# Optimization experiments

Measured on AMD Instinct MI355X. Metric: run time of the kernel, lower is better.

Reference implementation:

```python
import jax, jax.numpy as jnp
import numpy as np
import math

IN_DIM = 256
DQK = IN_DIM // 8


def setup_inputs() -> dict:
    key = jax.random.key(0)
    k = jax.random.split(key, 7)
    B, C, W = 4, IN_DIM, 4096
    x_0 = jax.random.normal(k[0], (B, C, W), dtype=jnp.float32)
    x_1 = jax.random.normal(k[1], (B, C, W), dtype=jnp.float32)
    s = 1.0 / math.sqrt(C)
    # 1x1 Conv1d == dense projection over channel dim: weight [out, in], bias [out]
    wq = jax.random.normal(k[2], (DQK, C), dtype=jnp.float32) * s
    bq = jax.random.normal(k[3], (DQK,), dtype=jnp.float32) * s
    wk = jax.random.normal(k[4], (DQK, C), dtype=jnp.float32) * s
    bk = jax.random.normal(k[5], (DQK,), dtype=jnp.float32) * s
    # torch init is zeros; use small random so the attention path contributes
    gamma = jax.random.normal(k[6], (1,), dtype=jnp.float32) * 0.1
    return {"x_0": x_0, "x_1": x_1, "wq": wq, "bq": bq, "wk": wk, "bk": bk, "gamma": gamma}


def reference(x_0, x_1, wq, bq, wk, bk, gamma):
    B, C, W0 = x_0.shape
    scale = 1.0 / math.sqrt(C)
    # 1x1 conv projections: [B, dqk, W]
    q = jnp.einsum('dc,bcw->bdw', wq, x_0) + bq[None, :, None]   # [B, dqk, W0]
    k = jnp.einsum('dc,bcw->bdw', wk, x_1) + bk[None, :, None]   # [B, dqk, W1]
    # energy = key^T @ query, scaled: [B, W1, W0]
    energy = jnp.einsum('bdm,bdn->bmn', k, q) * scale
    attention = jax.nn.softmax(energy, axis=-1)                  # softmax over W0
    # out = attention @ x_0^T -> [B, W1, C] -> permute to [B, C, W1]
    out = jnp.einsum('bmn,bcn->bcm', attention, x_0)
    out = gamma[0] * out + x_1
    return out, attention
```

## Files before the change

kernel.cpp:

```cpp
#include <hip/hip_runtime.h>
#include <stdint.h>

#define B_    4
#define C_    256
#define W_    4096
#define DQK_  32
#define NT64_ 64
#define TSZ_  16384

typedef short bf16x8 __attribute__((ext_vector_type(8)));
typedef float f32x4  __attribute__((ext_vector_type(4)));

__device__ __forceinline__ float fexp2f(float x){
#if __has_builtin(__builtin_amdgcn_exp2f)
  return __builtin_amdgcn_exp2f(x);
#else
  return exp2f(x);
#endif
}
__device__ __forceinline__ float frcpf(float x){
#if __has_builtin(__builtin_amdgcn_rcpf)
  return __builtin_amdgcn_rcpf(x);
#else
  return 1.0f / x;
#endif
}
__device__ __forceinline__ uint32_t cvtpk(float a, float b){
  uint32_t r;
  asm("v_cvt_pk_bf16_f32 %0, %1, %2" : "=v"(r) : "v"(a), "v"(b));
  return r;
}
__device__ __forceinline__ unsigned short bf16c(float f){
  return (unsigned short)cvtpk(f, f);
}

__global__ __launch_bounds__(512) void sa_prep(
    const float* __restrict__ x0, const float* __restrict__ x1,
    const float* __restrict__ wq, const float* __restrict__ bq,
    const float* __restrict__ wk, const float* __restrict__ bk,
    unsigned short* __restrict__ qf, unsigned short* __restrict__ kT,
    unsigned short* __restrict__ x0f)
{
  const int b    = blockIdx.y;
  const int nt   = blockIdx.x;
  const int tid  = threadIdx.x;
  const int lane = tid & 63;
  const int cq   = __builtin_amdgcn_readfirstlane(tid >> 6);
  const int n    = nt * 64 + lane;
  const int lr   = lane & 15, lg = lane >> 4;
  const size_t bw = (size_t)b * ((size_t)C_ * W_) + n;

  __shared__ union {
    unsigned short xs[256 * 68];
    float red[8][64][33];
  } sm;

  float accq[DQK_], acck[DQK_];
  #pragma unroll
  for (int d = 0; d < DQK_; ++d){ accq[d] = 0.f; acck[d] = 0.f; }

  const int c0 = cq * 32;
  for (int i = 0; i < 32; ++i){
    const int c = c0 + i;
    const size_t off = bw + (size_t)c * W_;
    const float v0 = x0[off];
    const float v1 = x1[off];
    sm.xs[c * 68 + lane] = bf16c(v0);
    #pragma unroll
    for (int d = 0; d < DQK_; ++d){
      accq[d] = fmaf(wq[d * C_ + c], v0, accq[d]);
      acck[d] = fmaf(wk[d * C_ + c], v1, acck[d]);
    }
  }

  {
    unsigned short* xt = x0f + (size_t)(b * NT64_ + nt) * TSZ_;
    #pragma unroll
    for (int ct = 0; ct < 2; ++ct)
      #pragma unroll
      for (int ks = 0; ks < 2; ++ks){
        uint4 v = *(const uint4*)&sm.xs[(c0 + ct * 16 + lr) * 68 + ks * 32 + lg * 8];
        *(uint4*)(xt + ((size_t)((cq * 2 + ct) * 2 + ks) * 64 + lane) * 8) = v;
      }
  }
  __syncthreads();

  #pragma unroll
  for (int d = 0; d < DQK_; ++d) sm.red[cq][lane][d] = accq[d];
  __syncthreads();
  {
    const int nl = tid & 63, dg = tid >> 6;
    const int d0 = dg * 4;
    float s[4];
    #pragma unroll
    for (int j = 0; j < 4; ++j){
      float t = bq[d0 + j];
      #pragma unroll
      for (int g = 0; g < 8; ++g) t += sm.red[g][nl][d0 + j];
      s[j] = t;
    }
    uint2 pk; pk.x = cvtpk(s[0], s[1]); pk.y = cvtpk(s[2], s[3]);
    const int ng = nt * 64 + nl;
    const size_t addr = (((size_t)b * 256 + (ng >> 4)) * 64
                         + (ng & 15) + ((dg >> 1) << 4)) * 8 + (dg & 1) * 4;
    *(uint2*)(qf + addr) = pk;
  }
  __syncthreads();

  #pragma unroll
  for (int d = 0; d < DQK_; ++d) sm.red[cq][lane][d] = acck[d];
  __syncthreads();
  {
    const float SCL = 0.0625f * 1.44269504088896340736f;
    const int nl = tid & 63, dg = tid >> 6;
    const int d0 = dg * 4;
    float s[4];
    #pragma unroll
    for (int j = 0; j < 4; ++j){
      float t = bk[d0 + j];
      #pragma unroll
      for (int g = 0; g < 8; ++g) t += sm.red[g][nl][d0 + j];
      s[j] = t * SCL;
    }
    uint2 pk; pk.x = cvtpk(s[0], s[1]); pk.y = cvtpk(s[2], s[3]);
    *(uint2*)(kT + ((size_t)b * W_ + nt * 64 + nl) * DQK_ + d0) = pk;
  }
}

__global__ __launch_bounds__(512, 2) void sa_fused(
    const unsigned short* __restrict__ qf, const unsigned short* __restrict__ kT,
    const unsigned short* __restrict__ x0f, const float* __restrict__ x1,
    const float* __restrict__ gamma,
    float* __restrict__ out, float* __restrict__ att)
{
  const int lb = blockIdx.x;
  const int b    = (lb & 7) >> 1;
  const int mblk = ((lb >> 3) << 1) | (lb & 1);
  const int m0 = mblk * 64;
  const int tid = threadIdx.x;
  const int lane = tid & 63;
  const int wid = tid >> 6;
  const int lr = lane & 15, lg = lane >> 4;
  const int nq = wid >> 1;
  const int mh = wid & 1;

  __shared__ __align__(16) unsigned short Plds[2][64 * 64];
  __shared__ float ssum[4][64];

  const int row0 = mh * 32 + lr, row1 = row0 + 16;
  const bf16x8 kf0 = *(const bf16x8*)(kT + ((size_t)b * W_ + m0 + row0) * DQK_ + lg * 8);
  const bf16x8 kf1 = *(const bf16x8*)(kT + ((size_t)b * W_ + m0 + row1) * DQK_ + lg * 8);
  const unsigned short* qfw = qf + ((size_t)b * 256 * 64 + (size_t)nq * 64 + lane) * 8;
  const unsigned short* afw = x0f + (size_t)b * NT64_ * TSZ_ + wid * 2048 + lane * 8;

  float ps0 = 0.f, ps1 = 0.f;
  {
    const unsigned short* qp = qfw + 2048;
    bf16x8 qv = *(const bf16x8*)qfw;
    for (int s = 0; s < NT64_; ++s){
      bf16x8 qn = *(const bf16x8*)qp;
      qp = (s == NT64_ - 2) ? qfw : (qp + 2048);
      f32x4 e0 = __builtin_amdgcn_mfma_f32_16x16x32_bf16(qv, kf0, (f32x4){0.f,0.f,0.f,0.f}, 0, 0, 0);
      f32x4 e1 = __builtin_amdgcn_mfma_f32_16x16x32_bf16(qv, kf1, (f32x4){0.f,0.f,0.f,0.f}, 0, 0, 0);
      ps0 += (fexp2f(e0[0]) + fexp2f(e0[1])) + (fexp2f(e0[2]) + fexp2f(e0[3]));
      ps1 += (fexp2f(e1[0]) + fexp2f(e1[1])) + (fexp2f(e1[2]) + fexp2f(e1[3]));
      qv = qn;
    }
  }
  ps0 += __shfl_xor(ps0, 16); ps0 += __shfl_xor(ps0, 32);
  ps1 += __shfl_xor(ps1, 16); ps1 += __shfl_xor(ps1, 32);
  if (lane < 16){
    ssum[nq][mh * 32 + lane]      = ps0;
    ssum[nq][mh * 32 + 16 + lane] = ps1;
  }
  __syncthreads();
  const float is0 = frcpf(ssum[0][row0] + ssum[1][row0] + ssum[2][row0] + ssum[3][row0]);
  const float is1 = frcpf(ssum[0][row1] + ssum[1][row1] + ssum[2][row1] + ssum[3][row1]);

  f32x4 acc[2][4];
  #pragma unroll
  for (int ct = 0; ct < 2; ++ct)
    #pragma unroll
    for (int m2 = 0; m2 < 4; ++m2) acc[ct][m2] = (f32x4){0.f,0.f,0.f,0.f};

  const int pw0 = row0 * 64 + (((nq * 2 + (lg >> 1)) ^ (row0 & 7)) << 3) + (lg & 1) * 4;
  const int pw1 = row1 * 64 + (((nq * 2 + (lg >> 1)) ^ (row1 & 7)) << 3) + (lg & 1) * 4;
  int pfo[4][2];
  #pragma unroll
  for (int m2 = 0; m2 < 4; ++m2){
    const int prow = m2 * 16 + lr;
    #pragma unroll
    for (int ks = 0; ks < 2; ++ks)
      pfo[m2][ks] = prow * 64 + (((ks * 4 + lg) ^ (prow & 7)) << 3);
  }

  const unsigned short* qp = qfw + 2048;
  const unsigned short* afp = afw + TSZ_;
  float* attw0 = att + ((size_t)b * W_ + m0 + row0) * W_ + nq * 16 + lg * 4;
  float* attw1 = attw0 + (size_t)16 * W_;

  bf16x8 qv = *(const bf16x8*)qfw;
  bf16x8 af0 = *(const bf16x8*)(afw);
  bf16x8 af1 = *(const bf16x8*)(afw + 512);
  bf16x8 af2 = *(const bf16x8*)(afw + 1024);
  bf16x8 af3 = *(const bf16x8*)(afw + 1536);

  for (int s = 0; s < NT64_; ++s){
    const int cur = s & 1;

    f32x4 e0 = __builtin_amdgcn_mfma_f32_16x16x32_bf16(qv, kf0, (f32x4){0.f,0.f,0.f,0.f}, 0, 0, 0);
    f32x4 e1 = __builtin_amdgcn_mfma_f32_16x16x32_bf16(qv, kf1, (f32x4){0.f,0.f,0.f,0.f}, 0, 0, 0);
    f32x4 p0, p1;
    #pragma unroll
    for (int r = 0; r < 4; ++r){
      p0[r] = fexp2f(e0[r]) * is0;
      p1[r] = fexp2f(e1[r]) * is1;
    }
    uint2 pv0; pv0.x = cvtpk(p0[0], p0[1]); pv0.y = cvtpk(p0[2], p0[3]);
    uint2 pv1; pv1.x = cvtpk(p1[0], p1[1]); pv1.y = cvtpk(p1[2], p1[3]);
    *(uint2*)(&Plds[cur][0] + pw0) = pv0;
    *(uint2*)(&Plds[cur][0] + pw1) = pv1;

    asm volatile("s_waitcnt lgkmcnt(0)" ::: "memory");
    __builtin_amdgcn_sched_barrier(0);
    __builtin_amdgcn_s_barrier();

    qv = *(const bf16x8*)qp;
    qp = (s == NT64_ - 2) ? qfw : (qp + 2048);
    bf16x8 an0 = *(const bf16x8*)(afp);
    bf16x8 an1 = *(const bf16x8*)(afp + 512);
    bf16x8 an2 = *(const bf16x8*)(afp + 1024);
    bf16x8 an3 = *(const bf16x8*)(afp + 1536);
    afp = (s == NT64_ - 2) ? afw : (afp + TSZ_);
    *(f32x4*)attw0 = p0;
    *(f32x4*)attw1 = p1;
    attw0 += 64; attw1 += 64;

    const unsigned short* Pb = &Plds[cur][0];
    bf16x8 pf[4][2];
    __builtin_amdgcn_s_setprio(1);
    #pragma unroll
    for (int m2 = 0; m2 < 4; ++m2)
      #pragma unroll
      for (int ks = 0; ks < 2; ++ks)
        pf[m2][ks] = *(const bf16x8*)(Pb + pfo[m2][ks]);
    #pragma unroll
    for (int m2 = 0; m2 < 4; ++m2){
      acc[0][m2] = __builtin_amdgcn_mfma_f32_16x16x32_bf16(af0, pf[m2][0], acc[0][m2], 0, 0, 0);
      acc[0][m2] = __builtin_amdgcn_mfma_f32_16x16x32_bf16(af1, pf[m2][1], acc[0][m2], 0, 0, 0);
      acc[1][m2] = __builtin_amdgcn_mfma_f32_16x16x32_bf16(af2, pf[m2][0], acc[1][m2], 0, 0, 0);
      acc[1][m2] = __builtin_amdgcn_mfma_f32_16x16x32_bf16(af3, pf[m2][1], acc[1][m2], 0, 0, 0);
    }
    __builtin_amdgcn_s_setprio(0);

    af0 = an0; af1 = an1; af2 = an2; af3 = an3;
  }

  const float g = gamma[0];
  const float* x1b = x1 + (size_t)b * C_ * W_;
  float* outb = out + (size_t)b * C_ * W_;
  #pragma unroll
  for (int ct = 0; ct < 2; ++ct)
    #pragma unroll
    for (int m2 = 0; m2 < 4; ++m2)
      #pragma unroll
      for (int r = 0; r < 4; ++r){
        const int c = wid * 32 + ct * 16 + lg * 4 + r;
        const size_t idx = (size_t)c * W_ + m0 + m2 * 16 + lr;
        outb[idx] = fmaf(g, acc[ct][m2][r], x1b[idx]);
      }
}

extern "C" void kernel_launch(void* const* d_in, const int* in_sizes, int n_in,
                              void* d_out, int out_size, void* d_ws, size_t ws_size,
                              hipStream_t stream)
{
  (void)in_sizes; (void)n_in; (void)out_size; (void)ws_size;
  const float* x0    = (const float*)d_in[0];
  const float* x1    = (const float*)d_in[1];
  const float* wq    = (const float*)d_in[2];
  const float* bq    = (const float*)d_in[3];
  const float* wk    = (const float*)d_in[4];
  const float* bk    = (const float*)d_in[5];
  const float* gamma = (const float*)d_in[6];

  unsigned short* qf  = (unsigned short*)d_ws;
  unsigned short* kT  = qf + (size_t)B_ * W_ * DQK_;
  unsigned short* x0f = kT + (size_t)B_ * W_ * DQK_;

  float* out = (float*)d_out;
  float* att = out + (size_t)B_ * C_ * W_;

  sa_prep <<<dim3(64, 4), 512, 0, stream>>>(x0, x1, wq, bq, wk, bk, qf, kT, x0f);
  sa_fused<<<256, 512, 0, stream>>>(qf, kT, x0f, x1, gamma, out, att);
}
```

Before: 127.1 us.

## Split key axis across waves with register-resident P via bpermute transpose

```diff
diff --git a/kernel.cpp b/kernel.cpp
--- a/kernel.cpp
+++ b/kernel.cpp
@@ -136,32 +136,34 @@
   const int lb = blockIdx.x;
   const int b    = (lb & 7) >> 1;
   const int mblk = ((lb >> 3) << 1) | (lb & 1);
-  const int m0 = mblk * 64;
+  const int m0 = mblk * 32;
   const int tid = threadIdx.x;
   const int lane = tid & 63;
   const int wid = tid >> 6;
+  const int nq = wid & 3;
+  const int ch = wid >> 2;
   const int lr = lane & 15, lg = lane >> 4;
-  const int nq = wid >> 1;
-  const int mh = wid & 1;
-
-  __shared__ __align__(16) unsigned short Plds[2][64 * 64];
-  __shared__ float ssum[4][64];
-
-  const int row0 = mh * 32 + lr, row1 = row0 + 16;
-  const bf16x8 kf0 = *(const bf16x8*)(kT + ((size_t)b * W_ + m0 + row0) * DQK_ + lg * 8);
-  const bf16x8 kf1 = *(const bf16x8*)(kT + ((size_t)b * W_ + m0 + row1) * DQK_ + lg * 8);
-  const unsigned short* qfw = qf + ((size_t)b * 256 * 64 + (size_t)nq * 64 + lane) * 8;
-  const unsigned short* afw = x0f + (size_t)b * NT64_ * TSZ_ + wid * 2048 + lane * 8;
+
+  __shared__ float ssum[8][32];
+  __shared__ __align__(16) float red[4][8][64][4];
+
+  const f32x4 z4 = {0.f, 0.f, 0.f, 0.f};
+  const bf16x8 kf0 = *(const bf16x8*)(kT + ((size_t)b * W_ + m0 + lr) * DQK_ + lg * 8);
+  const bf16x8 kf1 = *(const bf16x8*)(kT + ((size_t)b * W_ + m0 + 16 + lr) * DQK_ + lg * 8);
+
+  const unsigned short* qbase = qf + (size_t)b * 256 * 512 + (size_t)lane * 8;
+  const unsigned short* xbase = x0f + (size_t)b * NT64_ * TSZ_
+                                + (size_t)(ch * 16) * 512 + (size_t)lane * 8;
 
   float ps0 = 0.f, ps1 = 0.f;
   {
-    const unsigned short* qp = qfw + 2048;
-    bf16x8 qv = *(const bf16x8*)qfw;
-    for (int s = 0; s < NT64_; ++s){
-      bf16x8 qn = *(const bf16x8*)qp;
-      qp = (s == NT64_ - 2) ? qfw : (qp + 2048);
-      f32x4 e0 = __builtin_amdgcn_mfma_f32_16x16x32_bf16(qv, kf0, (f32x4){0.f,0.f,0.f,0.f}, 0, 0, 0);
-      f32x4 e1 = __builtin_amdgcn_mfma_f32_16x16x32_bf16(qv, kf1, (f32x4){0.f,0.f,0.f,0.f}, 0, 0, 0);
+    const unsigned short* qq = qbase + (size_t)(nq * 64) * 512;
+    bf16x8 qv = *(const bf16x8*)qq;
+    for (int i = 0; i < 64; ++i){
+      bf16x8 qn = *(const bf16x8*)(qq + 512);
+      qq += 512;
+      f32x4 e0 = __builtin_amdgcn_mfma_f32_16x16x32_bf16(qv, kf0, z4, 0, 0, 0);
+      f32x4 e1 = __builtin_amdgcn_mfma_f32_16x16x32_bf16(qv, kf1, z4, 0, 0, 0);
       ps0 += (fexp2f(e0[0]) + fexp2f(e0[1])) + (fexp2f(e0[2]) + fexp2f(e0[3]));
       ps1 += (fexp2f(e1[0]) + fexp2f(e1[1])) + (fexp2f(e1[2]) + fexp2f(e1[3]));
       qv = qn;
@@ -170,105 +172,164 @@
   ps0 += __shfl_xor(ps0, 16); ps0 += __shfl_xor(ps0, 32);
   ps1 += __shfl_xor(ps1, 16); ps1 += __shfl_xor(ps1, 32);
   if (lane < 16){
-    ssum[nq][mh * 32 + lane]      = ps0;
-    ssum[nq][mh * 32 + 16 + lane] = ps1;
-  }
-  __syncthreads();
-  const float is0 = frcpf(ssum[0][row0] + ssum[1][row0] + ssum[2][row0] + ssum[3][row0]);
-  const float is1 = frcpf(ssum[0][row1] + ssum[1][row1] + ssum[2][row1] + ssum[3][row1]);
-
-  f32x4 acc[2][4];
-  #pragma unroll
-  for (int ct = 0; ct < 2; ++ct)
-    #pragma unroll
-    for (int m2 = 0; m2 < 4; ++m2) acc[ct][m2] = (f32x4){0.f,0.f,0.f,0.f};
-
-  const int pw0 = row0 * 64 + (((nq * 2 + (lg >> 1)) ^ (row0 & 7)) << 3) + (lg & 1) * 4;
-  const int pw1 = row1 * 64 + (((nq * 2 + (lg >> 1)) ^ (row1 & 7)) << 3) + (lg & 1) * 4;
-  int pfo[4][2];
-  #pragma unroll
-  for (int m2 = 0; m2 < 4; ++m2){
-    const int prow = m2 * 16 + lr;
-    #pragma unroll
-    for (int ks = 0; ks < 2; ++ks)
-      pfo[m2][ks] = prow * 64 + (((ks * 4 + lg) ^ (prow & 7)) << 3);
-  }
-
-  const unsigned short* qp = qfw + 2048;
-  const unsigned short* afp = afw + TSZ_;
-  float* attw0 = att + ((size_t)b * W_ + m0 + row0) * W_ + nq * 16 + lg * 4;
+    ssum[wid][lane]      = ps0;
+    ssum[wid][16 + lane] = ps1;
+  }
+  __syncthreads();
+  const float is0 = frcpf(ssum[0][lr] + ssum[1][lr] + ssum[2][lr] + ssum[3][lr]);
+  const float is1 = frcpf(ssum[0][16 + lr] + ssum[1][16 + lr] + ssum[2][16 + lr] + ssum[3][16 + lr]);
+
+  f32x4 acc[8][2];
+  #pragma unroll
+  for (int ct = 0; ct < 8; ++ct){ acc[ct][0] = z4; acc[ct][1] = z4; }
+
+  const unsigned short* afp = xbase + (size_t)(nq * 16) * TSZ_;
+  bf16x8 afE[8], afO[8];
+  #pragma unroll
+  for (int ct = 0; ct < 8; ++ct) afE[ct] = *(const bf16x8*)(afp + (ct * 2 + 0) * 512);
+  #pragma unroll
+  for (int ct = 0; ct < 8; ++ct) afO[ct] = *(const bf16x8*)(afp + (ct * 2 + 1) * 512);
+
+  const unsigned short* qp = qbase + (size_t)(nq * 64) * 512;
+  bf16x8 qA0 = *(const bf16x8*)(qp);
+  bf16x8 qA1 = *(const bf16x8*)(qp + 512);
+  bf16x8 qB0 = *(const bf16x8*)(qp + 1024);
+  bf16x8 qB1 = *(const bf16x8*)(qp + 1536);
+
+  float* attw0 = att + ((size_t)b * W_ + m0 + lr) * W_ + nq * 1024 + lg * 4;
   float* attw1 = attw0 + (size_t)16 * W_;
 
-  bf16x8 qv = *(const bf16x8*)qfw;
-  bf16x8 af0 = *(const bf16x8*)(afw);
-  bf16x8 af1 = *(const bf16x8*)(afw + 512);
-  bf16x8 af2 = *(const bf16x8*)(afw + 1024);
-  bf16x8 af3 = *(const bf16x8*)(afw + 1536);
-
-  for (int s = 0; s < NT64_; ++s){
-    const int cur = s & 1;
-
-    f32x4 e0 = __builtin_amdgcn_mfma_f32_16x16x32_bf16(qv, kf0, (f32x4){0.f,0.f,0.f,0.f}, 0, 0, 0);
-    f32x4 e1 = __builtin_amdgcn_mfma_f32_16x16x32_bf16(qv, kf1, (f32x4){0.f,0.f,0.f,0.f}, 0, 0, 0);
-    f32x4 p0, p1;
-    #pragma unroll
-    for (int r = 0; r < 4; ++r){
-      p0[r] = fexp2f(e0[r]) * is0;
-      p1[r] = fexp2f(e1[r]) * is1;
-    }
-    uint2 pv0; pv0.x = cvtpk(p0[0], p0[1]); pv0.y = cvtpk(p0[2], p0[3]);
-    uint2 pv1; pv1.x = cvtpk(p1[0], p1[1]); pv1.y = cvtpk(p1[2], p1[3]);
-    *(uint2*)(&Plds[cur][0] + pw0) = pv0;
-    *(uint2*)(&Plds[cur][0] + pw1) = pv1;
-
-    asm volatile("s_waitcnt lgkmcnt(0)" ::: "memory");
-    __builtin_amdgcn_sched_barrier(0);
-    __builtin_amdgcn_s_barrier();
-
-    qv = *(const bf16x8*)qp;
-    qp = (s == NT64_ - 2) ? qfw : (qp + 2048);
-    bf16x8 an0 = *(const bf16x8*)(afp);
-    bf16x8 an1 = *(const bf16x8*)(afp + 512);
-    bf16x8 an2 = *(const bf16x8*)(afp + 1024);
-    bf16x8 an3 = *(const bf16x8*)(afp + 1536);
-    afp = (s == NT64_ - 2) ? afw : (afp + TSZ_);
-    *(f32x4*)attw0 = p0;
-    *(f32x4*)attw1 = p1;
+  const int sA = (lr + 32 * (lg & 1)) * 4;
+  const int sB = sA + 64;
+  const bool hi = (lg & 2) != 0;
+
+  #define TRANSPOSE_PF(PJ0, PJ1, PF)                                             \
+  {                                                                              \
+    const uint32_t c0 = cvtpk((PJ0)[0], (PJ0)[1]), c1 = cvtpk((PJ0)[2], (PJ0)[3]);\
+    const uint32_t c2 = cvtpk((PJ1)[0], (PJ1)[1]), c3 = cvtpk((PJ1)[2], (PJ1)[3]);\
+    const uint32_t a0 = (uint32_t)__builtin_amdgcn_ds_bpermute(sA, (int)c0);     \
+    const uint32_t a1 = (uint32_t)__builtin_amdgcn_ds_bpermute(sA, (int)c1);     \
+    const uint32_t a2 = (uint32_t)__builtin_amdgcn_ds_bpermute(sB, (int)c0);     \
+    const uint32_t a3 = (uint32_t)__builtin_amdgcn_ds_bpermute(sB, (int)c1);     \
+    const uint32_t b0 = (uint32_t)__builtin_amdgcn_ds_bpermute(sA, (int)c2);     \
+    const uint32_t b1 = (uint32_t)__builtin_amdgcn_ds_bpermute(sA, (int)c3);     \
+    const uint32_t b2 = (uint32_t)__builtin_amdgcn_ds_bpermute(sB, (int)c2);     \
+    const uint32_t b3 = (uint32_t)__builtin_amdgcn_ds_bpermute(sB, (int)c3);     \
+    union { uint32_t u[4]; bf16x8 v; } pfu_;                                     \
+    pfu_.u[0] = hi ? b0 : a0;                                                    \
+    pfu_.u[1] = hi ? b1 : a1;                                                    \
+    pfu_.u[2] = hi ? b2 : a2;                                                    \
+    pfu_.u[3] = hi ? b3 : a3;                                                    \
+    PF = pfu_.v;                                                                 \
+  }
+
+  for (int e = 0; e < 16; ++e){
+    const bool more = (e != 15);
+    {
+      f32x4 e00 = __builtin_amdgcn_mfma_f32_16x16x32_bf16(qA0, kf0, z4, 0, 0, 0);
+      f32x4 e01 = __builtin_amdgcn_mfma_f32_16x16x32_bf16(qA0, kf1, z4, 0, 0, 0);
+      f32x4 e10 = __builtin_amdgcn_mfma_f32_16x16x32_bf16(qA1, kf0, z4, 0, 0, 0);
+      f32x4 e11 = __builtin_amdgcn_mfma_f32_16x16x32_bf16(qA1, kf1, z4, 0, 0, 0);
+      if (more){
+        qA0 = *(const bf16x8*)(qp + 2048);
+        qA1 = *(const bf16x8*)(qp + 2048 + 512);
+      }
+      f32x4 p00, p01, p10, p11;
+      #pragma unroll
+      for (int r = 0; r < 4; ++r){
+        p00[r] = fexp2f(e00[r]) * is0;
+        p01[r] = fexp2f(e01[r]) * is1;
+        p10[r] = fexp2f(e10[r]) * is0;
+        p11[r] = fexp2f(e11[r]) * is1;
+      }
+      if (ch == 0){
+        *(f32x4*)(attw0)      = p00;
+        *(f32x4*)(attw0 + 16) = p10;
+        *(f32x4*)(attw1)      = p01;
+        *(f32x4*)(attw1 + 16) = p11;
+      }
+      bf16x8 pf0, pf1;
+      TRANSPOSE_PF(p00, p10, pf0);
+      TRANSPOSE_PF(p01, p11, pf1);
+      #pragma unroll
+      for (int ct = 0; ct < 8; ++ct){
+        acc[ct][0] = __builtin_amdgcn_mfma_f32_16x16x32_bf16(afE[ct], pf0, acc[ct][0], 0, 0, 0);
+        acc[ct][1] = __builtin_amdgcn_mfma_f32_16x16x32_bf16(afE[ct], pf1, acc[ct][1], 0, 0, 0);
+      }
+      if (more){
+        #pragma unroll
+        for (int ct = 0; ct < 8; ++ct)
+          afE[ct] = *(const bf16x8*)(afp + TSZ_ + (ct * 2 + 0) * 512);
+      }
+    }
+    {
+      f32x4 e00 = __builtin_amdgcn_mfma_f32_16x16x32_bf16(qB0, kf0, z4, 0, 0, 0);
+      f32x4 e01 = __builtin_amdgcn_mfma_f32_16x16x32_bf16(qB0, kf1, z4, 0, 0, 0);
+      f32x4 e10 = __builtin_amdgcn_mfma_f32_16x16x32_bf16(qB1, kf0, z4, 0, 0, 0);
+      f32x4 e11 = __builtin_amdgcn_mfma_f32_16x16x32_bf16(qB1, kf1, z4, 0, 0, 0);
+      if (more){
+        qB0 = *(const bf16x8*)(qp + 2048 + 1024);
+        qB1 = *(const bf16x8*)(qp + 2048 + 1536);
+      }
+      f32x4 p00, p01, p10, p11;
+      #pragma unroll
+      for (int r = 0; r < 4; ++r){
+        p00[r] = fexp2f(e00[r]) * is0;
+        p01[r] = fexp2f(e01[r]) * is1;
+        p10[r] = fexp2f(e10[r]) * is0;
+        p11[r] = fexp2f(e11[r]) * is1;
+      }
+      if (ch == 0){
+        *(f32x4*)(attw0 + 32) = p00;
+        *(f32x4*)(attw0 + 48) = p10;
+        *(f32x4*)(attw1 + 32) = p01;
+        *(f32x4*)(attw1 + 48) = p11;
+      }
+      bf16x8 pf0, pf1;
+      TRANSPOSE_PF(p00, p10, pf0);
+      TRANSPOSE_PF(p01, p11, pf1);
+      #pragma unroll
+      for (int ct = 0; ct < 8; ++ct){
+        acc[ct][0] = __builtin_amdgcn_mfma_f32_16x16x32_bf16(afO[ct], pf0, acc[ct][0], 0, 0, 0);
+        acc[ct][1] = __builtin_amdgcn_mfma_f32_16x16x32_bf16(afO[ct], pf1, acc[ct][1], 0, 0, 0);
+      }
+      if (more){
+        #pragma unroll
+        for (int ct = 0; ct < 8; ++ct)
+          afO[ct] = *(const bf16x8*)(afp + TSZ_ + (ct * 2 + 1) * 512);
+      }
+    }
+    qp += 2048;
+    afp += TSZ_;
     attw0 += 64; attw1 += 64;
-
-    const unsigned short* Pb = &Plds[cur][0];
-    bf16x8 pf[4][2];
-    __builtin_amdgcn_s_setprio(1);
-    #pragma unroll
-    for (int m2 = 0; m2 < 4; ++m2)
-      #pragma unroll
-      for (int ks = 0; ks < 2; ++ks)
-        pf[m2][ks] = *(const bf16x8*)(Pb + pfo[m2][ks]);
-    #pragma unroll
-    for (int m2 = 0; m2 < 4; ++m2){
-      acc[0][m2] = __builtin_amdgcn_mfma_f32_16x16x32_bf16(af0, pf[m2][0], acc[0][m2], 0, 0, 0);
-      acc[0][m2] = __builtin_amdgcn_mfma_f32_16x16x32_bf16(af1, pf[m2][1], acc[0][m2], 0, 0, 0);
-      acc[1][m2] = __builtin_amdgcn_mfma_f32_16x16x32_bf16(af2, pf[m2][0], acc[1][m2], 0, 0, 0);
-      acc[1][m2] = __builtin_amdgcn_mfma_f32_16x16x32_bf16(af3, pf[m2][1], acc[1][m2], 0, 0, 0);
-    }
-    __builtin_amdgcn_s_setprio(0);
-
-    af0 = an0; af1 = an1; af2 = an2; af3 = an3;
-  }
+  }
+  #undef TRANSPOSE_PF
 
   const float g = gamma[0];
   const float* x1b = x1 + (size_t)b * C_ * W_;
   float* outb = out + (size_t)b * C_ * W_;
   #pragma unroll
-  for (int ct = 0; ct < 2; ++ct)
-    #pragma unroll
-    for (int m2 = 0; m2 < 4; ++m2)
+  for (int mt = 0; mt < 2; ++mt){
+    #pragma unroll
+    for (int chR = 0; chR < 2; ++chR){
+      __syncthreads();
+      if (ch == chR){
+        #pragma unroll
+        for (int ct = 0; ct < 8; ++ct)
+          *(f32x4*)&red[nq][ct][lane][0] = acc[ct][mt];
+      }
+      __syncthreads();
+      f32x4 s = *(const f32x4*)&red[0][wid][lane][0];
+      #pragma unroll
+      for (int w = 1; w < 4; ++w) s += *(const f32x4*)&red[w][wid][lane][0];
       #pragma unroll
       for (int r = 0; r < 4; ++r){
-        const int c = wid * 32 + ct * 16 + lg * 4 + r;
-        const size_t idx = (size_t)c * W_ + m0 + m2 * 16 + lr;
-        outb[idx] = fmaf(g, acc[ct][m2][r], x1b[idx]);
-      }
+        const int c = (chR * 8 + wid) * 16 + lg * 4 + r;
+        const size_t idx = (size_t)c * W_ + m0 + mt * 16 + lr;
+        outb[idx] = fmaf(g, s[r], x1b[idx]);
+      }
+    }
+  }
 }
 
 extern "C" void kernel_launch(void* const* d_in, const int* in_sizes, int n_in,
@@ -292,5 +353,5 @@
   float* att = out + (size_t)B_ * C_ * W_;
 
   sa_prep <<<dim3(64, 4), 512, 0, stream>>>(x0, x1, wq, bq, wk, bk, qf, kT, x0f);
-  sa_fused<<<256, 512, 0, stream>>>(qf, kT, x0f, x1, gamma, out, att);
-}
+  sa_fused<<<512, 512, 0, stream>>>(qf, kT, x0f, x1, gamma, out, att);
+}
```

Result: slower. 143.2 us (+12.7%).
